# Kernel tuning notes

Measured on AMD Instinct MI355X. Metric: run time of the kernel, lower is better.

Reference implementation:

```python
import jax, jax.numpy as jnp
import numpy as np

T, B, C = 1024, 16, 1024
H, K, PAD_L = 16, 7, 3  # num_heads, kernel_size, padding_l
OUT = 1024


def setup_inputs() -> dict:
    key = jax.random.key(0)
    ks = jax.random.split(key, 8)
    s_in = 1.0 / np.sqrt(C)
    return {
        "x": jax.random.normal(ks[0], (T, B, C), dtype=jnp.float32),
        "W1": jax.random.normal(ks[1], (C, C), dtype=jnp.float32) * s_in,
        "b1": jnp.zeros((C,), dtype=jnp.float32),
        "Wq": jax.random.normal(ks[2], (C, H * K), dtype=jnp.float32) * s_in,
        "bq": jnp.zeros((H * K,), dtype=jnp.float32),
        "conv_bias": jax.random.normal(ks[3], (C,), dtype=jnp.float32) * 0.02,
        "W2": jax.random.normal(ks[4], (C, OUT), dtype=jnp.float32) * s_in,
        "b2": jnp.zeros((OUT,), dtype=jnp.float32),
    }


def reference(x, W1, b1, Wq, bq, conv_bias, W2, b2):
    # linear1 (glu=False -> no activation)
    h = x @ W1 + b1                       # [T, B, C]
    Tn, Bn, Cn = h.shape
    R = Cn // H                           # channels per head
    # dynamic filter prediction from query (= h), softmax over K taps
    w = (h @ Wq + bq).reshape(Tn, Bn, H, K)
    w = jax.nn.softmax(w, axis=-1)        # [T, B, H, K]
    # unfold1d: pad PAD_L left, K-1-PAD_L right along time, gather K-windows
    hp = jnp.pad(h, ((PAD_L, K - 1 - PAD_L), (0, 0), (0, 0)))
    win = jnp.stack([hp[k:k + Tn] for k in range(K)], axis=-1)  # [T, B, C, K]
    win = win.reshape(Tn, Bn, H, R, K)
    out = jnp.einsum('tbhrk,tbhk->tbhr', win, w).reshape(Tn, Bn, Cn)
    out = out + conv_bias                 # [T, B, C]
    return out @ W2 + b2                  # [T, B, OUT]
```

## Files before the change

### kernel.cpp

```cpp
#include <hip/hip_runtime.h>
#include <math.h>

#define T_DIM 1024
#define B_DIM 16
#define C_DIM 1024
#define H_DIM 16
#define K_TAPS 7
#define PAD_LEFT 3
#define OUT_DIM 1024
#define M_DIM (T_DIM * B_DIM)
#define HK 112
#define HKP 128
#define KD 1024

typedef __attribute__((ext_vector_type(8))) short bf16x8;
typedef __attribute__((ext_vector_type(4))) float f32x4;

__device__ __forceinline__ ushort f2bf(float f) {
    union { float f; unsigned u; } v; v.f = f;
    unsigned u = v.u;
    u += 0x7fffu + ((u >> 16) & 1u);
    return (ushort)(u >> 16);
}
__device__ __forceinline__ float bf2f(ushort h) {
    union { unsigned u; float f; } v; v.u = ((unsigned)h) << 16;
    return v.f;
}

__global__ __launch_bounds__(256) void cvt_bf16x8(const float* __restrict__ in,
                                                  ushort* __restrict__ out,
                                                  int n8) {
    int i = blockIdx.x * blockDim.x + threadIdx.x;
    if (i >= n8) return;
    const float4* p = (const float4*)in;
    float4 a = p[2 * i], b = p[2 * i + 1];
    uint4 o;
    o.x = (unsigned)f2bf(a.x) | ((unsigned)f2bf(a.y) << 16);
    o.y = (unsigned)f2bf(a.z) | ((unsigned)f2bf(a.w) << 16);
    o.z = (unsigned)f2bf(b.x) | ((unsigned)f2bf(b.y) << 16);
    o.w = (unsigned)f2bf(b.z) | ((unsigned)f2bf(b.w) << 16);
    ((uint4*)out)[i] = o;
}

__global__ void transpose_cvt(const float* __restrict__ W,
                              ushort* __restrict__ Wt,
                              int Kd, int N, int Npad) {
    __shared__ float tile[32][33];
    int n0 = blockIdx.x * 32, k0 = blockIdx.y * 32;
    int tx = threadIdx.x, ty = threadIdx.y;
#pragma unroll
    for (int j = 0; j < 4; ++j) {
        int k = k0 + ty * 4 + j;
        int n = n0 + tx;
        tile[ty * 4 + j][tx] = (n < N) ? W[(size_t)k * N + n] : 0.f;
    }
    __syncthreads();
#pragma unroll
    for (int j = 0; j < 4; ++j) {
        int n = n0 + ty * 4 + j;
        if (n < Npad)
            Wt[(size_t)n * Kd + k0 + tx] = f2bf(tile[tx][ty * 4 + j]);
    }
}

#define PHASE(P2KS, MH, READB, STAGE_STMT, VM_STMT)                           \
    {                                                                         \
        if (READB) {                                                          \
            _Pragma("unroll")                                                 \
            for (int n = 0; n < 4; ++n)                                       \
                b[n] = *(const bf16x8*)(Bbase + (P2KS)*8192 + bOff + n*512);  \
        }                                                                     \
        bf16x8 a_[4];                                                         \
        _Pragma("unroll")                                                     \
        for (int m = 0; m < 4; ++m)                                           \
            a_[m] = *(const bf16x8*)(Abase + (P2KS)*8192 + aOff +             \
                                     (MH)*2048 + m*512);                      \
        STAGE_STMT;                                                           \
        VM_STMT;                                                              \
        __builtin_amdgcn_s_barrier();                                         \
        asm volatile("s_waitcnt lgkmcnt(0)" ::: "memory");                    \
        __builtin_amdgcn_sched_barrier(0);                                    \
        __builtin_amdgcn_s_setprio(1);                                        \
        _Pragma("unroll")                                                     \
        for (int m = 0; m < 4; ++m)                                           \
            _Pragma("unroll")                                                 \
            for (int n = 0; n < 4; ++n)                                       \
                acc[(MH)*4 + m][n] = __builtin_amdgcn_mfma_f32_16x16x32_bf16( \
                    a_[m], b[n], acc[(MH)*4 + m][n], 0, 0, 0);                \
        __builtin_amdgcn_s_setprio(0);                                        \
        __builtin_amdgcn_s_barrier();                                         \
        __builtin_amdgcn_sched_barrier(0);                                    \
    }

template <bool OUT_BF16>
__global__ __launch_bounds__(512, 1) void gemm8p(
    const ushort* __restrict__ A, const ushort* __restrict__ Bt,
    const float* __restrict__ bias, void* __restrict__ Cp, int ldc) {
    __shared__ ushort Lds[8 * 8192];

    const int tid  = threadIdx.x;
    const int lane = tid & 63;
    const int wid  = tid >> 6;
    const int wr = wid >> 2;
    const int wc = wid & 3;
    const int fr = lane & 15;
    const int fq = lane >> 4;

    const int orig = blockIdx.x;
    const int nid  = (orig & 7) * 32 + (orig >> 3);
    const int bm = (nid >> 2) * 256;
    const int bn = (nid & 3) * 256;

    const int srow = tid >> 2;
    const int scol = ((tid & 3) ^ ((tid >> 3) & 3)) * 8;
    const size_t sA = (size_t)(bm + srow) * KD + scol;
    const size_t sB = (size_t)(bn + srow) * KD + scol;
    const int sdst = wid * 64 * 8;

    const int slotSw = (fq ^ ((fr >> 1) & 3)) * 8;
    const int aOff = (wr * 128 + fr) * 32 + slotSw;
    const int bOff = (wc * 64 + fr) * 32 + slotSw;
    const ushort* Abase = &Lds[0];
    const ushort* Bbase = &Lds[4 * 8192];

    f32x4 acc[8][4];
#pragma unroll
    for (int m = 0; m < 8; ++m)
#pragma unroll
        for (int n = 0; n < 4; ++n) acc[m][n] = (f32x4){0.f, 0.f, 0.f, 0.f};

    auto stageA = [&](int slot, int koff) {
#pragma unroll
        for (int i = 0; i < 2; ++i)
            __builtin_amdgcn_global_load_lds(
                (const __attribute__((address_space(1))) void*)(A + sA + koff + (size_t)i * 128 * KD),
                (__attribute__((address_space(3))) void*)(&Lds[slot * 8192 + i * 4096 + sdst]),
                16, 0, 0);
    };
    auto stageB = [&](int slot, int koff) {
#pragma unroll
        for (int i = 0; i < 2; ++i)
            __builtin_amdgcn_global_load_lds(
                (const __attribute__((address_space(1))) void*)(Bt + sB + koff + (size_t)i * 128 * KD),
                (__attribute__((address_space(3))) void*)(&Lds[(4 + slot) * 8192 + i * 4096 + sdst]),
                16, 0, 0);
    };

    stageA(0, 0);   stageB(0, 0);
    stageA(1, 32);  stageB(1, 32);
    stageA(2, 64);  stageB(2, 64);
    stageA(3, 96);  stageB(3, 96);
    asm volatile("s_waitcnt vmcnt(12)" ::: "memory");
    __builtin_amdgcn_sched_barrier(0);
    __builtin_amdgcn_s_barrier();
    __builtin_amdgcn_sched_barrier(0);

#pragma unroll 1
    for (int j = 0; j < 8; ++j) {
        bf16x8 b[4];
        const int e = 2 * j;

        PHASE(0, 0, 1,
              { if (j >= 1) stageA(3, (e + 1) * 64 + 32); },
              { asm volatile("s_waitcnt vmcnt(6)" ::: "memory");
                __builtin_amdgcn_sched_barrier(0); })
        PHASE(0, 1, 0,
              { if (j >= 1) stageB(3, (e + 1) * 64 + 32); },
              (void)0; )
        PHASE(1, 0, 1,
              { if (j < 7) stageA(0, (e + 2) * 64); },
              { if (j == 7) { asm volatile("s_waitcnt vmcnt(4)" ::: "memory"); }
                else        { asm volatile("s_waitcnt vmcnt(6)" ::: "memory"); }
                __builtin_amdgcn_sched_barrier(0); })
        PHASE(1, 1, 0,
              { if (j < 7) stageB(0, (e + 2) * 64); },
              (void)0; )
        PHASE(2, 0, 1,
              { if (j < 7) stageA(1, (e + 2) * 64 + 32); },
              { if (j == 7) { asm volatile("s_waitcnt vmcnt(0)" ::: "memory"); }
                else        { asm volatile("s_waitcnt vmcnt(6)" ::: "memory"); }
                __builtin_amdgcn_sched_barrier(0); })
        PHASE(2, 1, 0,
              { if (j < 7) stageB(1, (e + 2) * 64 + 32); },
              (void)0; )
        PHASE(3, 0, 1,
              { if (j < 7) stageA(2, (e + 3) * 64); },
              { asm volatile("s_waitcnt vmcnt(6)" ::: "memory");
                __builtin_amdgcn_sched_barrier(0); })
        PHASE(3, 1, 0,
              { if (j < 7) stageB(2, (e + 3) * 64); },
              (void)0; )
    }

#pragma unroll
    for (int n = 0; n < 4; ++n) {
        int col = bn + wc * 64 + n * 16 + fr;
        float bv = bias[col];
#pragma unroll
        for (int m = 0; m < 8; ++m) {
#pragma unroll
            for (int r = 0; r < 4; ++r) {
                int row = bm + wr * 128 + m * 16 + fq * 4 + r;
                float v = acc[m][n][r] + bv;
                if (OUT_BF16)
                    ((ushort*)Cp)[(size_t)row * ldc + col] = f2bf(v);
                else
                    ((float*)Cp)[(size_t)row * ldc + col] = v;
            }
        }
    }
}

template <bool OUT_BF16, bool NGUARD>
__global__ __launch_bounds__(256) void gemm_mfma(const ushort* __restrict__ A,
                                                 const ushort* __restrict__ Bt,
                                                 const float* __restrict__ bias,
                                                 void* __restrict__ Cp,
                                                 int Kd, int N, int ldc) {
    __shared__ ushort Als[128 * 32];
    __shared__ ushort Bls[128 * 32];
    const int tid  = threadIdx.x;
    const int lane = tid & 63;
    const int wid  = tid >> 6;
    const int wr = wid >> 1, wc = wid & 1;
    const int bm = blockIdx.y * 128, bn = blockIdx.x * 128;
    const int fq = lane >> 4, fr = lane & 15;

    f32x4 acc[4][4];
#pragma unroll
    for (int m = 0; m < 4; ++m)
#pragma unroll
        for (int n = 0; n < 4; ++n) acc[m][n] = (f32x4){0.f, 0.f, 0.f, 0.f};

    const int c0 = wid * 128 + lane;
    const int c1 = c0 + 64;
    const int r0 = c0 >> 2, o0 = (c0 & 3) * 8;
    const int r1 = c1 >> 2, o1 = (c1 & 3) * 8;

    for (int k0 = 0; k0 < Kd; k0 += 32) {
        __builtin_amdgcn_global_load_lds(
            (const __attribute__((address_space(1))) void*)&A[(size_t)(bm + r0) * Kd + k0 + o0],
            (__attribute__((address_space(3))) void*)&Als[(wid * 2 + 0) * 512], 16, 0, 0);
        __builtin_amdgcn_global_load_lds(
            (const __attribute__((address_space(1))) void*)&A[(size_t)(bm + r1) * Kd + k0 + o1],
            (__attribute__((address_space(3))) void*)&Als[(wid * 2 + 1) * 512], 16, 0, 0);
        __builtin_amdgcn_global_load_lds(
            (const __attribute__((address_space(1))) void*)&Bt[(size_t)(bn + r0) * Kd + k0 + o0],
            (__attribute__((address_space(3))) void*)&Bls[(wid * 2 + 0) * 512], 16, 0, 0);
        __builtin_amdgcn_global_load_lds(
            (const __attribute__((address_space(1))) void*)&Bt[(size_t)(bn + r1) * Kd + k0 + o1],
            (__attribute__((address_space(3))) void*)&Bls[(wid * 2 + 1) * 512], 16, 0, 0);
        __syncthreads();

        bf16x8 af[4], bfr[4];
#pragma unroll
        for (int m = 0; m < 4; ++m)
            af[m] = *(const bf16x8*)&Als[(wr * 64 + m * 16 + fr) * 32 + fq * 8];
#pragma unroll
        for (int n = 0; n < 4; ++n)
            bfr[n] = *(const bf16x8*)&Bls[(wc * 64 + n * 16 + fr) * 32 + fq * 8];
#pragma unroll
        for (int m = 0; m < 4; ++m)
#pragma unroll
            for (int n = 0; n < 4; ++n)
                acc[m][n] = __builtin_amdgcn_mfma_f32_16x16x32_bf16(
                    af[m], bfr[n], acc[m][n], 0, 0, 0);
        __syncthreads();
    }

#pragma unroll
    for (int m = 0; m < 4; ++m) {
#pragma unroll
        for (int n = 0; n < 4; ++n) {
            int col = bn + wc * 64 + n * 16 + fr;
            if (NGUARD && col >= N) continue;
            float bv = bias[col];
#pragma unroll
            for (int r = 0; r < 4; ++r) {
                int row = bm + wr * 64 + m * 16 + fq * 4 + r;
                float v = acc[m][n][r] + bv;
                if (OUT_BF16)
                    ((ushort*)Cp)[(size_t)row * ldc + col] = f2bf(v);
                else
                    ((float*)Cp)[(size_t)row * ldc + col] = v;
            }
        }
    }
}

__global__ __launch_bounds__(256) void dynconv_bf16(const ushort* __restrict__ h,
                                                    const float* __restrict__ q,
                                                    const float* __restrict__ cbias,
                                                    ushort* __restrict__ out) {
    const int m = blockIdx.x;
    const int t = m >> 4;
    const int b = m & 15;

    __shared__ float wsm[HK];
    if (threadIdx.x < HK)
        wsm[threadIdx.x] = q[(size_t)m * HK + threadIdx.x];
    __syncthreads();
    if (threadIdx.x < H_DIM) {
        float* p = &wsm[threadIdx.x * K_TAPS];
        float mx = p[0];
#pragma unroll
        for (int k = 1; k < K_TAPS; ++k) mx = fmaxf(mx, p[k]);
        float e[K_TAPS], s = 0.f;
#pragma unroll
        for (int k = 0; k < K_TAPS; ++k) { e[k] = __expf(p[k] - mx); s += e[k]; }
        float inv = 1.f / s;
#pragma unroll
        for (int k = 0; k < K_TAPS; ++k) p[k] = e[k] * inv;
    }
    __syncthreads();

    const int c = threadIdx.x * 4;
    const int hh = c >> 6;

    float4 bias = *(const float4*)&cbias[c];
    float a0 = bias.x, a1 = bias.y, a2 = bias.z, a3 = bias.w;

#pragma unroll
    for (int k = 0; k < K_TAPS; ++k) {
        int tt = t + k - PAD_LEFT;
        if (tt < 0 || tt >= T_DIM) continue;
        ushort4 hv = *(const ushort4*)&h[((size_t)tt * B_DIM + b) * C_DIM + c];
        float wk = wsm[hh * K_TAPS + k];
        a0 = fmaf(bf2f(hv.x), wk, a0);
        a1 = fmaf(bf2f(hv.y), wk, a1);
        a2 = fmaf(bf2f(hv.z), wk, a2);
        a3 = fmaf(bf2f(hv.w), wk, a3);
    }
    ushort4 o;
    o.x = f2bf(a0); o.y = f2bf(a1); o.z = f2bf(a2); o.w = f2bf(a3);
    *(ushort4*)&out[(size_t)m * C_DIM + c] = o;
}

extern "C" void kernel_launch(void* const* d_in, const int* in_sizes, int n_in,
                              void* d_out, int out_size, void* d_ws,
                              size_t ws_size, hipStream_t stream) {
    const float* x     = (const float*)d_in[0];
    const float* W1    = (const float*)d_in[1];
    const float* b1    = (const float*)d_in[2];
    const float* Wq    = (const float*)d_in[3];
    const float* bq    = (const float*)d_in[4];
    const float* cbias = (const float*)d_in[5];
    const float* W2    = (const float*)d_in[6];
    const float* b2    = (const float*)d_in[7];
    float* out = (float*)d_out;

    ushort* xb    = (ushort*)d_ws;
    ushort* hb    = xb    + (size_t)M_DIM * C_DIM;
    ushort* convb = hb    + (size_t)M_DIM * C_DIM;
    ushort* W1t   = convb + (size_t)M_DIM * C_DIM;
    ushort* W2t   = W1t   + (size_t)C_DIM * C_DIM;
    ushort* Wqt   = W2t   + (size_t)C_DIM * OUT_DIM;
    float*  q     = (float*)(Wqt + (size_t)HKP * C_DIM);

    cvt_bf16x8<<<dim3(M_DIM * C_DIM / 8 / 256), dim3(256), 0, stream>>>(
        x, xb, M_DIM * C_DIM / 8);
    transpose_cvt<<<dim3(C_DIM / 32, C_DIM / 32), dim3(32, 8), 0, stream>>>(
        W1, W1t, C_DIM, C_DIM, C_DIM);
    transpose_cvt<<<dim3(HKP / 32, C_DIM / 32), dim3(32, 8), 0, stream>>>(
        Wq, Wqt, C_DIM, HK, HKP);
    transpose_cvt<<<dim3(OUT_DIM / 32, C_DIM / 32), dim3(32, 8), 0, stream>>>(
        W2, W2t, C_DIM, OUT_DIM, OUT_DIM);

    gemm8p<true><<<dim3(256), dim3(512), 0, stream>>>(xb, W1t, b1, hb, C_DIM);

    gemm_mfma<false, true>
        <<<dim3(1, M_DIM / 128), dim3(256), 0, stream>>>(
            hb, Wqt, bq, q, C_DIM, HK, HK);

    dynconv_bf16<<<dim3(M_DIM), dim3(256), 0, stream>>>(hb, q, cbias, convb);

    gemm8p<false><<<dim3(256), dim3(512), 0, stream>>>(convb, W2t, b2, out,
                                                       OUT_DIM);
}
```

Baseline: 166.0 us.

## Tile dynamic conv over time in LDS, shrink q-GEMM tile, merge weight transposes

The dynamic convolution now processes 16 consecutive timesteps per block and stages a 22-row window of h in shared memory. Each h row is then fetched from global memory about once instead of seven times. The softmax is computed per (timestep, head) directly from q. The small q projection GEMM uses 64-row tiles, doubling block count for better occupancy, and the three weight transpose launches are merged into one to cut launch overhead. This adds larger LDS use per block (about 51KB), which may limit occupancy of the conv kernel.

New measurement: 150.3 us. -9.4%, faster.

```diff
diff --git a/kernel.cpp b/kernel.cpp
--- a/kernel.cpp
+++ b/kernel.cpp
@@ -42,11 +42,19 @@
     ((uint4*)out)[i] = o;
 }
 
-__global__ void transpose_cvt(const float* __restrict__ W,
-                              ushort* __restrict__ Wt,
-                              int Kd, int N, int Npad) {
+__global__ void transpose_all(const float* __restrict__ W1s,
+                              const float* __restrict__ Wqs,
+                              const float* __restrict__ W2s,
+                              ushort* __restrict__ W1t,
+                              ushort* __restrict__ Wqt,
+                              ushort* __restrict__ W2t) {
     __shared__ float tile[32][33];
-    int n0 = blockIdx.x * 32, k0 = blockIdx.y * 32;
+    int bx = blockIdx.x;
+    const float* W; ushort* Wt; int N, Npad, nb;
+    if (bx < 32)      { W = W1s; Wt = W1t; N = 1024; Npad = 1024; nb = bx; }
+    else if (bx < 36) { W = Wqs; Wt = Wqt; N = 112;  Npad = 128;  nb = bx - 32; }
+    else              { W = W2s; Wt = W2t; N = 1024; Npad = 1024; nb = bx - 36; }
+    int n0 = nb * 32, k0 = blockIdx.y * 32;
     int tx = threadIdx.x, ty = threadIdx.y;
 #pragma unroll
     for (int j = 0; j < 4; ++j) {
@@ -59,7 +67,7 @@
     for (int j = 0; j < 4; ++j) {
         int n = n0 + ty * 4 + j;
         if (n < Npad)
-            Wt[(size_t)n * Kd + k0 + tx] = f2bf(tile[tx][ty * 4 + j]);
+            Wt[(size_t)n * KD + k0 + tx] = f2bf(tile[tx][ty * 4 + j]);
     }
 }
 
@@ -211,56 +219,48 @@
     }
 }
 
-template <bool OUT_BF16, bool NGUARD>
-__global__ __launch_bounds__(256) void gemm_mfma(const ushort* __restrict__ A,
-                                                 const ushort* __restrict__ Bt,
-                                                 const float* __restrict__ bias,
-                                                 void* __restrict__ Cp,
-                                                 int Kd, int N, int ldc) {
-    __shared__ ushort Als[128 * 32];
+__global__ __launch_bounds__(256) void gemm_small(const ushort* __restrict__ A,
+                                                  const ushort* __restrict__ Bt,
+                                                  const float* __restrict__ bias,
+                                                  float* __restrict__ Cp) {
+    __shared__ ushort Als[64 * 32];
     __shared__ ushort Bls[128 * 32];
     const int tid  = threadIdx.x;
     const int lane = tid & 63;
     const int wid  = tid >> 6;
     const int wr = wid >> 1, wc = wid & 1;
-    const int bm = blockIdx.y * 128, bn = blockIdx.x * 128;
+    const int bm = blockIdx.y * 64;
     const int fq = lane >> 4, fr = lane & 15;
 
-    f32x4 acc[4][4];
-#pragma unroll
-    for (int m = 0; m < 4; ++m)
+    f32x4 acc[2][4];
+#pragma unroll
+    for (int m = 0; m < 2; ++m)
 #pragma unroll
         for (int n = 0; n < 4; ++n) acc[m][n] = (f32x4){0.f, 0.f, 0.f, 0.f};
 
-    const int c0 = wid * 128 + lane;
-    const int c1 = c0 + 64;
-    const int r0 = c0 >> 2, o0 = (c0 & 3) * 8;
-    const int r1 = c1 >> 2, o1 = (c1 & 3) * 8;
-
-    for (int k0 = 0; k0 < Kd; k0 += 32) {
+    const int rA = tid >> 2, oA = (tid & 3) * 8;
+    for (int k0 = 0; k0 < KD; k0 += 32) {
         __builtin_amdgcn_global_load_lds(
-            (const __attribute__((address_space(1))) void*)&A[(size_t)(bm + r0) * Kd + k0 + o0],
-            (__attribute__((address_space(3))) void*)&Als[(wid * 2 + 0) * 512], 16, 0, 0);
-        __builtin_amdgcn_global_load_lds(
-            (const __attribute__((address_space(1))) void*)&A[(size_t)(bm + r1) * Kd + k0 + o1],
-            (__attribute__((address_space(3))) void*)&Als[(wid * 2 + 1) * 512], 16, 0, 0);
-        __builtin_amdgcn_global_load_lds(
-            (const __attribute__((address_space(1))) void*)&Bt[(size_t)(bn + r0) * Kd + k0 + o0],
-            (__attribute__((address_space(3))) void*)&Bls[(wid * 2 + 0) * 512], 16, 0, 0);
-        __builtin_amdgcn_global_load_lds(
-            (const __attribute__((address_space(1))) void*)&Bt[(size_t)(bn + r1) * Kd + k0 + o1],
-            (__attribute__((address_space(3))) void*)&Bls[(wid * 2 + 1) * 512], 16, 0, 0);
+            (const __attribute__((address_space(1))) void*)&A[(size_t)(bm + rA) * KD + k0 + oA],
+            (__attribute__((address_space(3))) void*)&Als[wid * 64 * 8], 16, 0, 0);
+#pragma unroll
+        for (int i = 0; i < 2; ++i) {
+            int c = i * 256 + tid;
+            __builtin_amdgcn_global_load_lds(
+                (const __attribute__((address_space(1))) void*)&Bt[(size_t)(c >> 2) * KD + k0 + (c & 3) * 8],
+                (__attribute__((address_space(3))) void*)&Bls[(i * 256 + wid * 64) * 8], 16, 0, 0);
+        }
         __syncthreads();
 
-        bf16x8 af[4], bfr[4];
-#pragma unroll
-        for (int m = 0; m < 4; ++m)
-            af[m] = *(const bf16x8*)&Als[(wr * 64 + m * 16 + fr) * 32 + fq * 8];
+        bf16x8 af[2], bfr[4];
+#pragma unroll
+        for (int m = 0; m < 2; ++m)
+            af[m] = *(const bf16x8*)&Als[(wr * 32 + m * 16 + fr) * 32 + fq * 8];
 #pragma unroll
         for (int n = 0; n < 4; ++n)
             bfr[n] = *(const bf16x8*)&Bls[(wc * 64 + n * 16 + fr) * 32 + fq * 8];
 #pragma unroll
-        for (int m = 0; m < 4; ++m)
+        for (int m = 0; m < 2; ++m)
 #pragma unroll
             for (int n = 0; n < 4; ++n)
                 acc[m][n] = __builtin_amdgcn_mfma_f32_16x16x32_bf16(
@@ -269,39 +269,44 @@
     }
 
 #pragma unroll
-    for (int m = 0; m < 4; ++m) {
+    for (int m = 0; m < 2; ++m) {
 #pragma unroll
         for (int n = 0; n < 4; ++n) {
-            int col = bn + wc * 64 + n * 16 + fr;
-            if (NGUARD && col >= N) continue;
+            int col = wc * 64 + n * 16 + fr;
+            if (col >= HK) continue;
             float bv = bias[col];
 #pragma unroll
             for (int r = 0; r < 4; ++r) {
-                int row = bm + wr * 64 + m * 16 + fq * 4 + r;
-                float v = acc[m][n][r] + bv;
-                if (OUT_BF16)
-                    ((ushort*)Cp)[(size_t)row * ldc + col] = f2bf(v);
-                else
-                    ((float*)Cp)[(size_t)row * ldc + col] = v;
+                int row = bm + wr * 32 + m * 16 + fq * 4 + r;
+                Cp[(size_t)row * HK + col] = acc[m][n][r] + bv;
             }
         }
     }
 }
 
-__global__ __launch_bounds__(256) void dynconv_bf16(const ushort* __restrict__ h,
-                                                    const float* __restrict__ q,
-                                                    const float* __restrict__ cbias,
-                                                    ushort* __restrict__ out) {
-    const int m = blockIdx.x;
-    const int t = m >> 4;
-    const int b = m & 15;
-
-    __shared__ float wsm[HK];
-    if (threadIdx.x < HK)
-        wsm[threadIdx.x] = q[(size_t)m * HK + threadIdx.x];
-    __syncthreads();
-    if (threadIdx.x < H_DIM) {
-        float* p = &wsm[threadIdx.x * K_TAPS];
+__global__ __launch_bounds__(256) void dynconv2(const ushort* __restrict__ h,
+                                                const float* __restrict__ q,
+                                                const float* __restrict__ cbias,
+                                                ushort* __restrict__ out) {
+    __shared__ ushort hw[22][1024];
+    __shared__ float wsm[16][HK];
+    const int tid = threadIdx.x;
+    const int b  = blockIdx.x & 15;
+    const int t0 = (blockIdx.x >> 4) << 4;
+
+    for (int i = tid; i < 22 * 128; i += 256) {
+        int wrow = i >> 7;
+        int c8   = (i & 127) * 8;
+        int tt   = t0 + wrow - PAD_LEFT;
+        uint4 v = make_uint4(0, 0, 0, 0);
+        if (tt >= 0 && tt < T_DIM)
+            v = *(const uint4*)&h[((size_t)tt * B_DIM + b) * C_DIM + c8];
+        *(uint4*)&hw[wrow][c8] = v;
+    }
+    {
+        int tl = tid >> 4, hh = tid & 15;
+        int m = (t0 + tl) * B_DIM + b;
+        const float* p = &q[(size_t)m * HK + hh * K_TAPS];
         float mx = p[0];
 #pragma unroll
         for (int k = 1; k < K_TAPS; ++k) mx = fmaxf(mx, p[k]);
@@ -310,30 +315,29 @@
         for (int k = 0; k < K_TAPS; ++k) { e[k] = __expf(p[k] - mx); s += e[k]; }
         float inv = 1.f / s;
 #pragma unroll
-        for (int k = 0; k < K_TAPS; ++k) p[k] = e[k] * inv;
+        for (int k = 0; k < K_TAPS; ++k) wsm[tl][hh * K_TAPS + k] = e[k] * inv;
     }
     __syncthreads();
 
-    const int c = threadIdx.x * 4;
+    const int c  = tid * 4;
     const int hh = c >> 6;
-
     float4 bias = *(const float4*)&cbias[c];
-    float a0 = bias.x, a1 = bias.y, a2 = bias.z, a3 = bias.w;
-
-#pragma unroll
-    for (int k = 0; k < K_TAPS; ++k) {
-        int tt = t + k - PAD_LEFT;
-        if (tt < 0 || tt >= T_DIM) continue;
-        ushort4 hv = *(const ushort4*)&h[((size_t)tt * B_DIM + b) * C_DIM + c];
-        float wk = wsm[hh * K_TAPS + k];
-        a0 = fmaf(bf2f(hv.x), wk, a0);
-        a1 = fmaf(bf2f(hv.y), wk, a1);
-        a2 = fmaf(bf2f(hv.z), wk, a2);
-        a3 = fmaf(bf2f(hv.w), wk, a3);
-    }
-    ushort4 o;
-    o.x = f2bf(a0); o.y = f2bf(a1); o.z = f2bf(a2); o.w = f2bf(a3);
-    *(ushort4*)&out[(size_t)m * C_DIM + c] = o;
+
+    for (int tl = 0; tl < 16; ++tl) {
+        float a0 = bias.x, a1 = bias.y, a2 = bias.z, a3 = bias.w;
+#pragma unroll
+        for (int k = 0; k < K_TAPS; ++k) {
+            ushort4 hv = *(const ushort4*)&hw[tl + k][c];
+            float wk = wsm[tl][hh * K_TAPS + k];
+            a0 = fmaf(bf2f(hv.x), wk, a0);
+            a1 = fmaf(bf2f(hv.y), wk, a1);
+            a2 = fmaf(bf2f(hv.z), wk, a2);
+            a3 = fmaf(bf2f(hv.w), wk, a3);
+        }
+        ushort4 o;
+        o.x = f2bf(a0); o.y = f2bf(a1); o.z = f2bf(a2); o.w = f2bf(a3);
+        *(ushort4*)&out[((size_t)(t0 + tl) * B_DIM + b) * C_DIM + c] = o;
+    }
 }
 
 extern "C" void kernel_launch(void* const* d_in, const int* in_sizes, int n_in,
@@ -359,20 +363,15 @@
 
     cvt_bf16x8<<<dim3(M_DIM * C_DIM / 8 / 256), dim3(256), 0, stream>>>(
         x, xb, M_DIM * C_DIM / 8);
-    transpose_cvt<<<dim3(C_DIM / 32, C_DIM / 32), dim3(32, 8), 0, stream>>>(
-        W1, W1t, C_DIM, C_DIM, C_DIM);
-    transpose_cvt<<<dim3(HKP / 32, C_DIM / 32), dim3(32, 8), 0, stream>>>(
-        Wq, Wqt, C_DIM, HK, HKP);
-    transpose_cvt<<<dim3(OUT_DIM / 32, C_DIM / 32), dim3(32, 8), 0, stream>>>(
-        W2, W2t, C_DIM, OUT_DIM, OUT_DIM);
+    transpose_all<<<dim3(68, 32), dim3(32, 8), 0, stream>>>(
+        W1, Wq, W2, W1t, Wqt, W2t);
 
     gemm8p<true><<<dim3(256), dim3(512), 0, stream>>>(xb, W1t, b1, hb, C_DIM);
 
-    gemm_mfma<false, true>
-        <<<dim3(1, M_DIM / 128), dim3(256), 0, stream>>>(
-            hb, Wqt, bq, q, C_DIM, HK, HK);
-
-    dynconv_bf16<<<dim3(M_DIM), dim3(256), 0, stream>>>(hb, q, cbias, convb);
+    gemm_small<<<dim3(1, M_DIM / 64), dim3(256), 0, stream>>>(hb, Wqt, bq, q);
+
+    dynconv2<<<dim3(B_DIM * T_DIM / 16), dim3(256), 0, stream>>>(
+        hb, q, cbias, convb);
 
     gemm8p<false><<<dim3(256), dim3(512), 0, stream>>>(convb, W2t, b2, out,
                                                        OUT_DIM);
```
